# Performance work log

Measured on AMD Instinct MI355X. Metric: run time of the kernel, lower is better.

## Reference

```python
import jax, jax.numpy as jnp
import numpy as np

B, NUM_ATOMS, NUM_CHANNELS, MAX_L = 4, 4096, 32, 3


def setup_inputs() -> dict:
    key = jax.random.key(0)
    ks = jax.random.split(key, MAX_L + 1)
    inp = {}
    for l in range(MAX_L + 1):
        # parts[l]: [b, num_atoms, 1, 2l+1, num_channels]
        inp[f"part{l}"] = jax.random.normal(
            ks[l], (B, NUM_ATOMS, 1, 2 * l + 1, NUM_CHANNELS), dtype=jnp.float32
        )
    return inp


def reference(part0, part1, part2, part3):
    b, a = part0.shape[0], part0.shape[1]
    c = part0.shape[-1]
    # scalars_part0: reshape of l=0 part -> [b, atoms, C]
    scalars0 = part0.reshape(b, a, c)
    # SO(3)-invariant norm: per-l channel Gram matrix reduced over the m axis.
    # Ordering matches the torch loop: l-major, channel1-major, channel2-minor.
    grams = []
    for p in (part0, part1, part2, part3):
        g = jnp.einsum("banmc,banmd->bacd", p, p)  # [b, atoms, C, C]
        grams.append(g.reshape(b, a, c * c))
    return jnp.concatenate([scalars0] + grams, axis=-1)  # [b, atoms, C + (max_l+1)*C^2]
```

## Files before the change

### kernel.cpp

```cpp
#include <hip/hip_runtime.h>


constexpr int C = 32;
constexpr int OUT_PER_ATOM = C + 4 * C * C;
constexpr int APB = 8;

typedef float f32x4 __attribute__((ext_vector_type(4)));

template <int R0, int NM>
__device__ __forceinline__ f32x4 gram4(const float* __restrict__ L, int c, int d) {
    f32x4 acc = {0.f, 0.f, 0.f, 0.f};
    #pragma unroll
    for (int m = 0; m < NM; ++m) {
        const float* row = L + (R0 + m) * C;
        const float pc = row[c];
        const f32x4 pd = *reinterpret_cast<const f32x4*>(row + d);
        acc += pc * pd;
    }
    return acc;
}

__global__ __launch_bounds__(256) void getscalars_kernel(
    const float* __restrict__ p0, const float* __restrict__ p1,
    const float* __restrict__ p2, const float* __restrict__ p3,
    float* __restrict__ out)
{
    __shared__ float lds[APB * 16 * C];

    const int t = threadIdx.x;
    const int atom0 = blockIdx.x * APB;

    #pragma unroll
    for (int s = 0; s < 4; ++s) {
        const int j = t + s * 256;
        const int a = j >> 7;
        const int k = j & 127;
        const int atom = atom0 + a;
        const f32x4* src;
        int idx;
        if (k < 8)       { src = (const f32x4*)(p0 + (size_t)atom * 32);  idx = k; }
        else if (k < 32) { src = (const f32x4*)(p1 + (size_t)atom * 96);  idx = k - 8; }
        else if (k < 72) { src = (const f32x4*)(p2 + (size_t)atom * 160); idx = k - 32; }
        else             { src = (const f32x4*)(p3 + (size_t)atom * 224); idx = k - 72; }
        reinterpret_cast<f32x4*>(lds)[j] = src[idx];
    }
    __syncthreads();

    const int c = t >> 3;
    const int d = (t & 7) * 4;

    for (int a = 0; a < APB; ++a) {
        const float* L = lds + a * 16 * C;
        float* outp = out + (size_t)(atom0 + a) * OUT_PER_ATOM;

        if (t < 8) {
            __builtin_nontemporal_store(reinterpret_cast<const f32x4*>(L)[t],
                                        reinterpret_cast<f32x4*>(outp) + t);
        }

        __builtin_nontemporal_store(gram4<0, 1>(L, c, d),
            reinterpret_cast<f32x4*>(outp + C + 0 * 1024 + 4 * t));
        __builtin_nontemporal_store(gram4<1, 3>(L, c, d),
            reinterpret_cast<f32x4*>(outp + C + 1 * 1024 + 4 * t));
        __builtin_nontemporal_store(gram4<4, 5>(L, c, d),
            reinterpret_cast<f32x4*>(outp + C + 2 * 1024 + 4 * t));
        __builtin_nontemporal_store(gram4<9, 7>(L, c, d),
            reinterpret_cast<f32x4*>(outp + C + 3 * 1024 + 4 * t));
    }
}

extern "C" void kernel_launch(void* const* d_in, const int* in_sizes, int n_in,
                              void* d_out, int out_size, void* d_ws, size_t ws_size,
                              hipStream_t stream) {
    const float* p0 = (const float*)d_in[0];
    const float* p1 = (const float*)d_in[1];
    const float* p2 = (const float*)d_in[2];
    const float* p3 = (const float*)d_in[3];
    float* out = (float*)d_out;

    const int natoms = in_sizes[0] / C;
    getscalars_kernel<<<natoms / APB, 256, 0, stream>>>(p0, p1, p2, p3, out);
}
```

Before: 58.86 us.

## Assign one wave per angular momentum level in Gram computation

Each wavefront now computes the full Gram matrix for one l level, with every lane producing four 4-wide rows, where before all 256 threads computed one 4-wide piece for every level. This reuses each loaded pd vector across four accumulators, which cuts LDS reads per output. Atoms per block drop from 8 to 4, launch bounds ask for 6 blocks per CU, and nontemporal stores become normal stores. Work is now unbalanced across waves because the l=3 wave does seven m iterations and the l=0 wave does one, so the slowest wave limits each atom.

```diff
diff --git a/kernel.cpp b/kernel.cpp
--- a/kernel.cpp
+++ b/kernel.cpp
@@ -3,24 +3,36 @@
 
 constexpr int C = 32;
 constexpr int OUT_PER_ATOM = C + 4 * C * C;
-constexpr int APB = 8;
+constexpr int APB = 4;
 
 typedef float f32x4 __attribute__((ext_vector_type(4)));
 
-template <int R0, int NM>
-__device__ __forceinline__ f32x4 gram4(const float* __restrict__ L, int c, int d) {
-    f32x4 acc = {0.f, 0.f, 0.f, 0.f};
+template <int LV>
+__device__ __forceinline__ void gram_wave(const float* __restrict__ Lp,
+                                          int lane, float* __restrict__ outp) {
+    constexpr int R0 = LV * LV;
+    constexpr int NM = 2 * LV + 1;
+    const int dq = (lane & 7) * 4;
+    const int c0 = lane >> 3;
+
+    f32x4 a0 = {0.f, 0.f, 0.f, 0.f}, a1 = a0, a2 = a0, a3 = a0;
     #pragma unroll
     for (int m = 0; m < NM; ++m) {
-        const float* row = L + (R0 + m) * C;
-        const float pc = row[c];
-        const f32x4 pd = *reinterpret_cast<const f32x4*>(row + d);
-        acc += pc * pd;
+        const float* row = Lp + (R0 + m) * C;
+        const f32x4 pd = *reinterpret_cast<const f32x4*>(row + dq);
+        a0 += row[c0     ] * pd;
+        a1 += row[c0 +  8] * pd;
+        a2 += row[c0 + 16] * pd;
+        a3 += row[c0 + 24] * pd;
     }
-    return acc;
+    float* gbase = outp + C + LV * 1024;
+    *reinterpret_cast<f32x4*>(gbase + (c0     ) * C + dq) = a0;
+    *reinterpret_cast<f32x4*>(gbase + (c0 +  8) * C + dq) = a1;
+    *reinterpret_cast<f32x4*>(gbase + (c0 + 16) * C + dq) = a2;
+    *reinterpret_cast<f32x4*>(gbase + (c0 + 24) * C + dq) = a3;
 }
 
-__global__ __launch_bounds__(256) void getscalars_kernel(
+__global__ __launch_bounds__(256, 6) void getscalars_kernel(
     const float* __restrict__ p0, const float* __restrict__ p1,
     const float* __restrict__ p2, const float* __restrict__ p3,
     float* __restrict__ out)
@@ -31,7 +43,7 @@
     const int atom0 = blockIdx.x * APB;
 
     #pragma unroll
-    for (int s = 0; s < 4; ++s) {
+    for (int s = 0; s < 2; ++s) {
         const int j = t + s * 256;
         const int a = j >> 7;
         const int k = j & 127;
@@ -46,26 +58,26 @@
     }
     __syncthreads();
 
-    const int c = t >> 3;
-    const int d = (t & 7) * 4;
+    const int w = t >> 6;
+    const int lane = t & 63;
 
     for (int a = 0; a < APB; ++a) {
-        const float* L = lds + a * 16 * C;
+        const float* Lp = lds + a * 16 * C;
         float* outp = out + (size_t)(atom0 + a) * OUT_PER_ATOM;
 
-        if (t < 8) {
-            __builtin_nontemporal_store(reinterpret_cast<const f32x4*>(L)[t],
-                                        reinterpret_cast<f32x4*>(outp) + t);
+        if (w == 0) {
+            if (lane < 8) {
+                reinterpret_cast<f32x4*>(outp)[lane] =
+                    reinterpret_cast<const f32x4*>(Lp)[lane];
+            }
+            gram_wave<0>(Lp, lane, outp);
+        } else if (w == 1) {
+            gram_wave<1>(Lp, lane, outp);
+        } else if (w == 2) {
+            gram_wave<2>(Lp, lane, outp);
+        } else {
+            gram_wave<3>(Lp, lane, outp);
         }
-
-        __builtin_nontemporal_store(gram4<0, 1>(L, c, d),
-            reinterpret_cast<f32x4*>(outp + C + 0 * 1024 + 4 * t));
-        __builtin_nontemporal_store(gram4<1, 3>(L, c, d),
-            reinterpret_cast<f32x4*>(outp + C + 1 * 1024 + 4 * t));
-        __builtin_nontemporal_store(gram4<4, 5>(L, c, d),
-            reinterpret_cast<f32x4*>(outp + C + 2 * 1024 + 4 * t));
-        __builtin_nontemporal_store(gram4<9, 7>(L, c, d),
-            reinterpret_cast<f32x4*>(outp + C + 3 * 1024 + 4 * t));
     }
 }
 
```

Result: faster. 55.32 us (-6.0%).
